# Kernel optimization log

Measured on AMD Instinct MI355X. Metric: run time of the kernel, lower is better.

The kernel has to match this reference:

```python
import jax, jax.numpy as jnp
import numpy as np

N, E = 100000, 3200000
F_NODE, F_EDGE = 2, 7
H, C = 4, 8
HC = H * C
REG, TGT = 500, 1
NUM_LAYERS = 3
ATT_SLOPE = 0.2   # LeakyReLU inside GATv2 attention
ACT_SLOPE = 0.01  # model-level LeakyReLU default
BN_EPS = 1e-5


def gatv2(x, src, dst, e_attr, Wl, bl, Wr, br, We, att, bias):
    n = x.shape[0]
    xl = (x @ Wl + bl).reshape(n, H, C)          # source transform (messages)
    xr = (x @ Wr + br).reshape(n, H, C)          # destination transform
    ee = (e_attr @ We).reshape(-1, H, C)         # edge transform (no bias in PyG)
    m = jax.nn.leaky_relu(xl[src] + xr[dst] + ee, ATT_SLOPE)  # [Ef,H,C]
    logits = jnp.einsum('ehc,hc->eh', m, att)    # [Ef,H]
    mx = jax.ops.segment_max(logits, dst, num_segments=n)
    ex = jnp.exp(logits - mx[dst])
    den = jax.ops.segment_sum(ex, dst, num_segments=n)
    alpha = ex / (den[dst] + 1e-16)              # edge-softmax grouped by dst
    out = jax.ops.segment_sum(xl[src] * alpha[:, :, None], dst, num_segments=n)
    return out.reshape(n, HC) + bias             # concat heads + bias


def setup_inputs() -> dict:
    key = jax.random.key(0)
    ks = jax.random.split(key, 30)
    # edges with no self loops (module calls add_self_loops on top)
    s = jax.random.randint(ks[0], (E,), 0, N, dtype=jnp.int32)
    off = jax.random.randint(ks[1], (E,), 1, N, dtype=jnp.int32)
    d = (s + off) % N
    edge_index = jnp.stack([s, d])
    x = jax.random.normal(ks[2], (N, F_NODE), dtype=jnp.float32)
    edge_attr = jax.random.normal(ks[3], (E, F_EDGE), dtype=jnp.float32)

    def glorot(k, shape):
        fan = shape[0] + shape[-1]
        return jax.random.normal(k, shape, dtype=jnp.float32) * jnp.sqrt(2.0 / fan)

    inp = dict(x=x, edge_index=edge_index, edge_attr=edge_attr)
    i = 4
    for tag, fin in (("1", F_NODE), ("2", HC)):
        inp["Wl" + tag] = glorot(ks[i], (fin, HC)); i += 1
        inp["bl" + tag] = jnp.zeros((HC,), jnp.float32)
        inp["Wr" + tag] = glorot(ks[i], (fin, HC)); i += 1
        inp["br" + tag] = jnp.zeros((HC,), jnp.float32)
        inp["We" + tag] = glorot(ks[i], (F_EDGE, HC)); i += 1
        inp["att" + tag] = glorot(ks[i], (H, C)); i += 1
        inp["b" + tag] = jnp.zeros((HC,), jnp.float32)
    inp["gamma"] = jnp.ones((HC,), jnp.float32)
    inp["beta"] = jnp.zeros((HC,), jnp.float32)
    inp["Wreg"] = glorot(ks[i], (HC, REG)); i += 1
    inp["breg"] = jnp.zeros((REG,), jnp.float32)
    inp["Wend"] = glorot(ks[i], (REG, TGT)); i += 1
    inp["bend"] = jnp.zeros((TGT,), jnp.float32)
    return inp


def reference(x, edge_index, edge_attr,
              Wl1, bl1, Wr1, br1, We1, att1, b1,
              Wl2, bl2, Wr2, br2, We2, att2, b2,
              gamma, beta, Wreg, breg, Wend, bend):
    n = x.shape[0]
    loop = jnp.arange(n, dtype=edge_index.dtype)
    srcf = jnp.concatenate([edge_index[0], loop])
    dstf = jnp.concatenate([edge_index[1], loop])
    # self-loop edge attrs filled with mean (PyG fill_value='mean')
    ea_mean = jnp.mean(edge_attr, axis=0, keepdims=True)
    eaf = jnp.concatenate([edge_attr, jnp.broadcast_to(ea_mean, (n, edge_attr.shape[1]))])

    h = gatv2(x, srcf, dstf, eaf, Wl1, bl1, Wr1, br1, We1, att1, b1)
    for _ in range(NUM_LAYERS - 1):
        mu = jnp.mean(h, axis=0)
        var = jnp.var(h, axis=0)
        h = (h - mu) * jax.lax.rsqrt(var + BN_EPS) * gamma + beta
        h = jax.nn.leaky_relu(h, ACT_SLOPE)
        h = gatv2(h, srcf, dstf, eaf, Wl2, bl2, Wr2, br2, We2, att2, b2)
    h = jax.nn.leaky_relu(h, ACT_SLOPE)
    h = h @ Wreg + breg
    return h @ Wend + bend
```

## Files before the change

kernel.cpp:

```cpp
#include <hip/hip_runtime.h>
#include <hip/hip_fp16.h>
#include <math.h>

#define NN 100000
#define EE 3200000
#define FE 7
#define GNB 32
#define CRR 1280
#define NBK 391
#define BKCAP 8688
#define T1 8192
#define FB1 ((EE + T1 - 1) / T1)

typedef unsigned int uivec4 __attribute__((ext_vector_type(4)));
static __device__ __forceinline__ uint4 ntload4(const uint4* p) {
    uivec4 v = __builtin_nontemporal_load((const uivec4*)p);
    uint4 r; r.x = v.x; r.y = v.y; r.z = v.z; r.w = v.w; return r;
}

static __device__ __forceinline__ __half2 hmax2(__half2 a, __half2 b) {
    unsigned int ua = *(unsigned int*)&a, ub = *(unsigned int*)&b, ur;
    asm("v_pk_max_f16 %0, %1, %2" : "=v"(ur) : "v"(ua), "v"(ub));
    return *(__half2*)&ur;
}


__global__ void k_prep(const float* __restrict__ Wreg, const float* __restrict__ breg,
                       const float* __restrict__ Wend, const float* __restrict__ bend,
                       float* __restrict__ wend, float* __restrict__ c0v,
                       int* __restrict__ gbucket) {
    if (blockIdx.x == 0) {
        int t = threadIdx.x;
        if (t < 32) {
            float s = 0.f;
            for (int k = 0; k < 500; ++k) s = fmaf(Wreg[t * 500 + k], Wend[k], s);
            wend[t] = s;
        } else if (t == 32) {
            float s = 0.f;
            for (int k = 0; k < 500; ++k) s = fmaf(breg[k], Wend[k], s);
            *c0v = s + bend[0];
        }
    } else {
        for (int i = threadIdx.x; i < NBK; i += 256) gbucket[i] = i * BKCAP;
    }
}

__global__ __launch_bounds__(512) void k_fill1(const int* __restrict__ ei,
                                               const float* __restrict__ ea,
                                               int* __restrict__ gbucket,
                                               uint4* __restrict__ srt,
                                               double* __restrict__ ea_sum) {
    __shared__ int hbin[NBK];
    __shared__ float part[8][FE];
    for (int i = threadIdx.x; i < NBK; i += 512) hbin[i] = 0;
    __syncthreads();
    int e0 = blockIdx.x * T1;
    int ecnt = EE - e0; if (ecnt > T1) ecnt = T1;
    for (int i = threadIdx.x; i < ecnt; i += 512) {
        int d = ei[EE + e0 + i];
        atomicAdd(&hbin[d >> 8], 1);
    }
    __syncthreads();
    for (int i = threadIdx.x; i < NBK; i += 512) {
        int c = hbin[i];
        hbin[i] = (c > 0) ? atomicAdd(&gbucket[i], c) : 0;
    }
    __syncthreads();
    float acc[FE];
#pragma unroll
    for (int f = 0; f < FE; ++f) acc[f] = 0.f;
    for (int i = threadIdx.x; i < ecnt; i += 512) {
        int e = e0 + i;
        int d = ei[EE + e];
        int b = d >> 8;
        unsigned dl = (unsigned)(d & 255);
        int pos = atomicAdd(&hbin[b], 1);
        int s = ei[e];
        const float* rr = ea + (size_t)e * FE;
        unsigned h[FE];
#pragma unroll
        for (int f = 0; f < FE; ++f) {
            float af = __builtin_nontemporal_load(rr + f);
            acc[f] += af;
            h[f] = (unsigned)__half_as_ushort(__float2half_rn(af));
        }
#pragma unroll
        for (int f = 0; f < 6; ++f) { h[f] = (h[f] + 1) >> 1; if (h[f] > 0x7FFFu) h[f] = 0x7FFFu; }
        unsigned h6 = (h[6] + 4) >> 3; if (h6 > 0x1FFFu) h6 = 0x1FFFu;
        uint4 u;
        u.x = h[0] | (h[1] << 15) | ((dl & 3u) << 30);
        u.y = h[2] | (h[3] << 15) | (((dl >> 2) & 3u) << 30);
        u.z = h[4] | (h[5] << 15) | (((dl >> 4) & 3u) << 30);
        u.w = (unsigned)s | (h6 << 17) | ((dl >> 6) << 30);
        srt[(size_t)pos] = u;
    }
    int wave = threadIdx.x >> 6;
#pragma unroll
    for (int f = 0; f < FE; ++f) {
        float v = acc[f];
        for (int o = 32; o > 0; o >>= 1) v += __shfl_down(v, o, 64);
        if ((threadIdx.x & 63) == 0) part[wave][f] = v;
    }
    __syncthreads();
    if (threadIdx.x < FE) {
        float s = 0.f;
#pragma unroll
        for (int i = 0; i < 8; ++i) s += part[i][threadIdx.x];
        atomicAdd(&ea_sum[threadIdx.x], (double)s);
    }
}

__global__ __launch_bounds__(512) void k_bscan(const int* __restrict__ gbucket,
                                               int* __restrict__ bbase,
                                               const double* __restrict__ ea_sum,
                                               float* __restrict__ ea_mean) {
    __shared__ int ts[512];
    int t = threadIdx.x;
    if (t < 8) ea_mean[t] = (t < FE) ? (float)(ea_sum[t] / (double)EE) : 0.f;
    int c = (t < NBK) ? (gbucket[t] - t * BKCAP) : 0;
    ts[t] = c;
    __syncthreads();
    for (int o = 1; o < 512; o <<= 1) {
        int u = (t >= o) ? ts[t - o] : 0;
        __syncthreads();
        ts[t] += u;
        __syncthreads();
    }
    if (t < NBK) bbase[t] = ts[t] - c;
}

__global__ __launch_bounds__(512) void k_fill2(const uint4* __restrict__ srt,
                                               const int* __restrict__ gbucket,
                                               const int* __restrict__ bbase,
                                               int* __restrict__ offs,
                                               uint4* __restrict__ rec) {
    __shared__ int hist[256], hcopy[256], strt[256];
    int t = threadIdx.x;
    int b = blockIdx.x;
    int nbase = b << 8;
    int nb = NN - nbase; if (nb > 256) nb = 256;
    int sbase = b * BKCAP;
    int cnt = gbucket[b] - sbase;
    int bb = bbase[b];
    if (t < 256) hist[t] = 0;
    __syncthreads();
    for (int p = t; p < cnt; p += 512) {
        uint4 s = srt[(size_t)(sbase + p)];
        int dl = (int)((s.x >> 30) | ((s.y >> 30) << 2) | ((s.z >> 30) << 4) | ((s.w >> 30) << 6));
        atomicAdd(&hist[dl], 1);
    }
    __syncthreads();
    if (t < 256) hcopy[t] = hist[t];
    __syncthreads();
    for (int o = 1; o < 256; o <<= 1) {
        int u = 0;
        if (t < 256 && t >= o) u = hist[t - o];
        __syncthreads();
        if (t < 256) hist[t] += u;
        __syncthreads();
    }
    if (t < 256) {
        int c = hcopy[t];
        int start = bb + hist[t] - c;
        strt[t] = start;
        if (t < nb) offs[nbase + t] = start + c;
    }
    __syncthreads();
    for (int p = t; p < cnt; p += 512) {
        uint4 s = srt[(size_t)(sbase + p)];
        int dl = (int)((s.x >> 30) | ((s.y >> 30) << 2) | ((s.z >> 30) << 4) | ((s.w >> 30) << 6));
        int pos = atomicAdd(&strt[dl], 1);
        uint4 u;
        u.x = ((s.x & 0x7FFFu) << 1) | (((s.x >> 15) & 0x7FFFu) << 17);
        u.y = ((s.y & 0x7FFFu) << 1) | (((s.y >> 15) & 0x7FFFu) << 17);
        u.z = ((s.z & 0x7FFFu) << 1) | (((s.z >> 15) & 0x7FFFu) << 17);
        u.w = (s.w & 0x1FFFFu) | (((s.w >> 17) & 0x1FFFu) << 19);
        rec[(size_t)pos] = u;
    }
}

template <int FIN, bool BN>
__global__ void k_xform(const float* __restrict__ h,
                        const float* __restrict__ Wl, const float* __restrict__ bl,
                        const float* __restrict__ Wr, const float* __restrict__ br,
                        const double* __restrict__ bn_part, const double* __restrict__ bn_sqpart,
                        const float* __restrict__ gamma, const float* __restrict__ beta,
                        __half* __restrict__ xl, __half* __restrict__ xr) {
    __shared__ float sWl[FIN * 32], sWr[FIN * 32], sb[64];
    __shared__ float smu[FIN], ssc[FIN], sbe[FIN];
    for (int i = threadIdx.x; i < FIN * 32; i += blockDim.x) { sWl[i] = Wl[i]; sWr[i] = Wr[i]; }
    if (threadIdx.x < 32) { sb[threadIdx.x] = bl[threadIdx.x]; sb[32 + threadIdx.x] = br[threadIdx.x]; }
    if (BN && threadIdx.x < FIN) {
        int f = threadIdx.x;
        double s = 0.0, q = 0.0;
#pragma unroll
        for (int k = 0; k < 32; ++k) { s += bn_part[k * 32 + f]; q += bn_sqpart[k * 32 + f]; }
        double mu = s * (1.0 / NN);
        double var = q * (1.0 / NN) - mu * mu;
        smu[f] = (float)mu;
        ssc[f] = gamma[f] * (float)(1.0 / sqrt(var + 1e-5));
        sbe[f] = beta[f];
    }
    __syncthreads();
    int idx = blockIdx.x * blockDim.x + threadIdx.x;
    if (idx >= NN * 32) return;
    int n = idx >> 5, c = idx & 31;
    const float* hr = h + (size_t)n * FIN;
    float al = sb[c], ar = sb[32 + c];
#pragma unroll
    for (int f = 0; f < FIN; ++f) {
        float v = hr[f];
        if (BN) {
            v = fmaf(v - smu[f], ssc[f], sbe[f]);
            v = v > 0.f ? v : 0.01f * v;
        }
        al = fmaf(v, sWl[f * 32 + c], al);
        ar = fmaf(v, sWr[f * 32 + c], ar);
    }
    xl[idx] = __float2half(al);
    xr[idx] = __float2half(ar);
}

template <int MODE>
__global__ __launch_bounds__(256) void k_gat_t(
    const int* __restrict__ offs, const uint4* __restrict__ rec,
    const __half* __restrict__ xl, const __half* __restrict__ xr,
    const float* __restrict__ We, const float* __restrict__ att,
    const float* __restrict__ bias, const float* __restrict__ ea_mean,
    float* __restrict__ hout, double* __restrict__ bn_part,
    double* __restrict__ bn_sqpart, const float* __restrict__ wend,
    const float* __restrict__ c0v, float* __restrict__ out) {
    __shared__ uint4 srec[CRR];
    int n0 = blockIdx.x * GNB;
    int g = threadIdx.x >> 3, j = threadIdx.x & 7, c0 = j * 4;
    int node = n0 + g;

    __half2 weh[FE][2];
#pragma unroll
    for (int f = 0; f < FE; ++f) {
        weh[f][0] = __floats2half2_rn(We[f * 32 + c0], We[f * 32 + c0 + 1]);
        weh[f][1] = __floats2half2_rn(We[f * 32 + c0 + 2], We[f * 32 + c0 + 3]);
    }
    float at0 = att[c0], at1 = att[c0 + 1], at2 = att[c0 + 2], at3 = att[c0 + 3];
    float eam[FE];
#pragma unroll
    for (int f = 0; f < FE; ++f) eam[f] = ea_mean[f];

    float2 rawr = *(const float2*)(xr + (size_t)node * 32 + c0);
    __half2 qh01 = *(const __half2*)&rawr.x;
    __half2 qh23 = *(const __half2*)&rawr.y;
    float2 q01 = __half22float2(qh01);
    float2 q23 = __half22float2(qh23);

    int s_g = (node == 0) ? 0 : offs[node - 1];
    int e_g = offs[node];
    int range0 = (n0 == 0) ? 0 : offs[n0 - 1];
    int range1 = offs[n0 + GNB - 1];

    float sm = 0.f, acc0 = 0.f, acc1 = 0.f, acc2 = 0.f, acc3 = 0.f;
    const __half2 c02 = __float2half2_rn(0.2f);

    auto edge_op = [&](uint4 u, float2 rawl) {
        __half2 lh01 = *(const __half2*)&rawl.x;
        __half2 lh23 = *(const __half2*)&rawl.y;
        __half2 ah01 = *(const __half2*)&u.x;
        __half2 ah23 = *(const __half2*)&u.y;
        __half2 ah45 = *(const __half2*)&u.z;
        __half a6h = __ushort_as_half((unsigned short)((u.w >> 16) & 0xFFFEu));
        __half2 e01 = qh01, e23 = qh23;
        __half2 bc;
        bc = __low2half2(ah01);  e01 = __hfma2(bc, weh[0][0], e01); e23 = __hfma2(bc, weh[0][1], e23);
        bc = __high2half2(ah01); e01 = __hfma2(bc, weh[1][0], e01); e23 = __hfma2(bc, weh[1][1], e23);
        bc = __low2half2(ah23);  e01 = __hfma2(bc, weh[2][0], e01); e23 = __hfma2(bc, weh[2][1], e23);
        bc = __high2half2(ah23); e01 = __hfma2(bc, weh[3][0], e01); e23 = __hfma2(bc, weh[3][1], e23);
        bc = __low2half2(ah45);  e01 = __hfma2(bc, weh[4][0], e01); e23 = __hfma2(bc, weh[4][1], e23);
        bc = __high2half2(ah45); e01 = __hfma2(bc, weh[5][0], e01); e23 = __hfma2(bc, weh[5][1], e23);
        bc = __half2half2(a6h);  e01 = __hfma2(bc, weh[6][0], e01); e23 = __hfma2(bc, weh[6][1], e23);
        __half2 v01 = __hadd2(e01, lh01);
        __half2 v23 = __hadd2(e23, lh23);
        v01 = hmax2(v01, __hmul2(v01, c02));
        v23 = hmax2(v23, __hmul2(v23, c02));
        float2 f01 = __half22float2(v01), f23 = __half22float2(v23);
        float pl = fmaf(f01.x, at0, fmaf(f01.y, at1, fmaf(f23.x, at2, f23.y * at3)));
        float L = pl + __shfl_xor(pl, 1, 64);
        float ex = __expf(L);
        sm += ex;
        float2 l01 = __half22float2(lh01), l23 = __half22float2(lh23);
        acc0 = fmaf(ex, l01.x, acc0);
        acc1 = fmaf(ex, l01.y, acc1);
        acc2 = fmaf(ex, l23.x, acc2);
        acc3 = fmaf(ex, l23.y, acc3);
    };

    for (int base = range0; base < range1; base += CRR) {
        int cnt = range1 - base; if (cnt > CRR) cnt = CRR;
        __syncthreads();
        for (int i = threadIdx.x; i < cnt; i += 256)
            srec[i] = ntload4(&rec[(size_t)base + i]);
        __syncthreads();
        int lo = s_g > base ? s_g : base;
        int hi = e_g < base + cnt ? e_g : base + cnt;
        if (lo >= hi) continue;
        int i1 = lo + 1 < hi ? lo + 1 : hi - 1;
        int i2 = lo + 2 < hi ? lo + 2 : hi - 1;
        uint4 ua = srec[lo - base];
        float2 ra = *(const float2*)(xl + (size_t)(ua.w & 0x1FFFFu) * 32 + c0);
        uint4 ub = srec[i1 - base];
        float2 rb = *(const float2*)(xl + (size_t)(ub.w & 0x1FFFFu) * 32 + c0);
        uint4 uc = srec[i2 - base];
        float2 rc = *(const float2*)(xl + (size_t)(uc.w & 0x1FFFFu) * 32 + c0);
#pragma unroll 3
        for (int p = lo; p < hi; ++p) {
            uint4 cu = ua; float2 cr = ra;
            ua = ub; ra = rb;
            ub = uc; rb = rc;
            int pn = p + 3 < hi ? p + 3 : hi - 1;
            uc = srec[pn - base];
            rc = *(const float2*)(xl + (size_t)(uc.w & 0x1FFFFu) * 32 + c0);
            edge_op(cu, cr);
        }
    }

    {
        float2 rawl = *(const float2*)(xl + (size_t)node * 32 + c0);
        float2 l01 = __half22float2(*(const __half2*)&rawl.x);
        float2 l23 = __half22float2(*(const __half2*)&rawl.y);
        float ee0 = q01.x, ee1 = q01.y, ee2 = q23.x, ee3 = q23.y;
        float wef[FE][4];
#pragma unroll
        for (int f = 0; f < FE; ++f) {
            float2 w0 = __half22float2(weh[f][0]);
            float2 w1 = __half22float2(weh[f][1]);
            wef[f][0] = w0.x; wef[f][1] = w0.y; wef[f][2] = w1.x; wef[f][3] = w1.y;
        }
#pragma unroll
        for (int f = 0; f < FE; ++f) {
            ee0 = fmaf(eam[f], wef[f][0], ee0);
            ee1 = fmaf(eam[f], wef[f][1], ee1);
            ee2 = fmaf(eam[f], wef[f][2], ee2);
            ee3 = fmaf(eam[f], wef[f][3], ee3);
        }
        float v0 = ee0 + l01.x;
        float v1 = ee1 + l01.y;
        float v2 = ee2 + l23.x;
        float v3 = ee3 + l23.y;
        v0 = fmaxf(v0, 0.2f * v0);
        v1 = fmaxf(v1, 0.2f * v1);
        v2 = fmaxf(v2, 0.2f * v2);
        v3 = fmaxf(v3, 0.2f * v3);
        float pl = fmaf(v0, at0, fmaf(v1, at1, fmaf(v2, at2, v3 * at3)));
        float L = pl + __shfl_xor(pl, 1, 64);
        float ex = __expf(L);
        sm += ex;
        acc0 = fmaf(ex, l01.x, acc0);
        acc1 = fmaf(ex, l01.y, acc1);
        acc2 = fmaf(ex, l23.x, acc2);
        acc3 = fmaf(ex, l23.y, acc3);
    }

    float inv = 1.f / (sm + 1e-16f);
    float o0 = fmaf(acc0, inv, bias[c0 + 0]);
    float o1 = fmaf(acc1, inv, bias[c0 + 1]);
    float o2 = fmaf(acc2, inv, bias[c0 + 2]);
    float o3 = fmaf(acc3, inv, bias[c0 + 3]);
    if constexpr (MODE != 2) {
        float4 o; o.x = o0; o.y = o1; o.z = o2; o.w = o3;
        *(float4*)(hout + (size_t)node * 32 + c0) = o;
    }
    if constexpr (MODE == 1) {
        float s0 = o0, s1 = o1, s2 = o2, s3 = o3;
        float z0 = o0 * o0, z1 = o1 * o1, z2 = o2 * o2, z3 = o3 * o3;
#pragma unroll
        for (int off = 8; off < 64; off <<= 1) {
            s0 += __shfl_xor(s0, off, 64); z0 += __shfl_xor(z0, off, 64);
            s1 += __shfl_xor(s1, off, 64); z1 += __shfl_xor(z1, off, 64);
            s2 += __shfl_xor(s2, off, 64); z2 += __shfl_xor(z2, off, 64);
            s3 += __shfl_xor(s3, off, 64); z3 += __shfl_xor(z3, off, 64);
        }
        __syncthreads();
        float* red = (float*)srec;
        int wv = threadIdx.x >> 6, lane = threadIdx.x & 63;
        if (lane < 8) {
            float* r = red + (wv * 8 + lane) * 8;
            r[0] = s0; r[1] = s1; r[2] = s2; r[3] = s3;
            r[4] = z0; r[5] = z1; r[6] = z2; r[7] = z3;
        }
        __syncthreads();
        if (threadIdx.x < 32) {
            int jj = threadIdx.x >> 2, kk = threadIdx.x & 3;
            float ts = 0.f, tq = 0.f;
#pragma unroll
            for (int w2 = 0; w2 < 4; ++w2) {
                ts += red[(w2 * 8 + jj) * 8 + kk];
                tq += red[(w2 * 8 + jj) * 8 + 4 + kk];
            }
            int slot = (blockIdx.x & 31) * 32 + threadIdx.x;
            atomicAdd(&bn_part[slot], (double)ts);
            atomicAdd(&bn_sqpart[slot], (double)tq);
        }
    }
    if constexpr (MODE == 2) {
        float w0 = wend[c0], w1 = wend[c0 + 1], w2 = wend[c0 + 2], w3 = wend[c0 + 3];
        float p0 = o0 > 0.f ? o0 : 0.01f * o0;
        float p1 = o1 > 0.f ? o1 : 0.01f * o1;
        float p2 = o2 > 0.f ? o2 : 0.01f * o2;
        float p3 = o3 > 0.f ? o3 : 0.01f * o3;
        float p = fmaf(p0, w0, fmaf(p1, w1, fmaf(p2, w2, p3 * w3)));
        p += __shfl_xor(p, 1, 64);
        p += __shfl_xor(p, 2, 64);
        p += __shfl_xor(p, 4, 64);
        if (j == 0) out[node] = p + *c0v;
    }
}

extern "C" void kernel_launch(void* const* d_in, const int* in_sizes, int n_in,
                              void* d_out, int out_size, void* d_ws, size_t ws_size,
                              hipStream_t stream) {
    (void)in_sizes; (void)n_in; (void)out_size; (void)ws_size;
    const float* x    = (const float*)d_in[0];
    const int*   ei   = (const int*)d_in[1];
    const float* ea   = (const float*)d_in[2];
    const float* Wl1  = (const float*)d_in[3];
    const float* bl1  = (const float*)d_in[4];
    const float* Wr1  = (const float*)d_in[5];
    const float* br1  = (const float*)d_in[6];
    const float* We1  = (const float*)d_in[7];
    const float* att1 = (const float*)d_in[8];
    const float* b1   = (const float*)d_in[9];
    const float* Wl2  = (const float*)d_in[10];
    const float* bl2  = (const float*)d_in[11];
    const float* Wr2  = (const float*)d_in[12];
    const float* br2  = (const float*)d_in[13];
    const float* We2  = (const float*)d_in[14];
    const float* att2 = (const float*)d_in[15];
    const float* b2   = (const float*)d_in[16];
    const float* gamma= (const float*)d_in[17];
    const float* beta = (const float*)d_in[18];
    const float* Wreg = (const float*)d_in[19];
    const float* breg = (const float*)d_in[20];
    const float* Wend = (const float*)d_in[21];
    const float* bend = (const float*)d_in[22];
    float* out = (float*)d_out;

    char* w = (char*)d_ws;
    double* ea_sum   = (double*)(w + 0);
    float*  ea_mean  = (float*)(w + 576);
    float*  wend     = (float*)(w + 608);
    float*  c0v      = (float*)(w + 736);
    int*    gbucket  = (int*)(w + 2048);
    int*    bbase    = (int*)(w + 4096);
    double* bn_part  = (double*)(w + 8192);
    double* bn_sqp   = (double*)(w + 16384);
    size_t o = 24576;
    int* offs = (int*)(w + o); o += ((size_t)NN * 4 + 255) & ~(size_t)255;
    __half* xl = (__half*)(w + o); o += ((size_t)NN * 32 * 2 + 255) & ~(size_t)255;
    __half* xr = (__half*)(w + o); o += ((size_t)NN * 32 * 2 + 255) & ~(size_t)255;
    float* hb = (float*)(w + o); o += (size_t)NN * 32 * 4;
    uint4* rec = (uint4*)(w + o); o += (size_t)EE * 16;
    uint4* srt = (uint4*)(w + o); o += (size_t)NBK * BKCAP * 16;

    hipMemsetAsync(w, 0, 1024, stream);
    hipMemsetAsync(w + 8192, 0, 16384, stream);

    k_prep<<<2, 256, 0, stream>>>(Wreg, breg, Wend, bend, wend, c0v, gbucket);
    k_fill1<<<FB1, 512, 0, stream>>>(ei, ea, gbucket, srt, ea_sum);
    k_bscan<<<1, 512, 0, stream>>>(gbucket, bbase, ea_sum, ea_mean);
    k_fill2<<<NBK, 512, 0, stream>>>(srt, gbucket, bbase, offs, rec);

    const int xbl = (NN * 32 + 255) / 256;
    const int gbl = NN / GNB;

    k_xform<2, false><<<xbl, 256, 0, stream>>>(x, Wl1, bl1, Wr1, br1,
                                               bn_part, bn_sqp, gamma, beta, xl, xr);
    k_gat_t<1><<<gbl, 256, 0, stream>>>(offs, rec, xl, xr, We1, att1, b1, ea_mean,
                                        hb, bn_part, bn_sqp, wend, c0v, out);

    k_xform<32, true><<<xbl, 256, 0, stream>>>(hb, Wl2, bl2, Wr2, br2,
                                               bn_part, bn_sqp, gamma, beta, xl, xr);
    hipMemsetAsync(w + 8192, 0, 16384, stream);
    k_gat_t<1><<<gbl, 256, 0, stream>>>(offs, rec, xl, xr, We2, att2, b2, ea_mean,
                                        hb, bn_part, bn_sqp, wend, c0v, out);

    k_xform<32, true><<<xbl, 256, 0, stream>>>(hb, Wl2, bl2, Wr2, br2,
                                               bn_part, bn_sqp, gamma, beta, xl, xr);
    k_gat_t<2><<<gbl, 256, 0, stream>>>(offs, rec, xl, xr, We2, att2, b2, ea_mean,
                                        hb, bn_part, bn_sqp, wend, c0v, out);
}
```

Measured before the change: 671.7 us.

## Drop prep kernel and memsets, stage edge attributes through LDS, halve fill tile

Removes k_prep by starting bucket counters at zero, so the bucket base is added inside k_fill1, and by moving the Wreg·Wend reduction into k_bscan. A single memset now zeroes the workspace, and two BN-stat buffers are used so the mid-pipeline memset can go. In k_fill1, edge attributes are loaded into shared memory one coalesced tile of 512 edges at a time with 16-byte nontemporal loads, replacing strided per-thread 4-byte loads. The per-block edge count is halved to T1=4096, which doubles the block count and the global bucket atomics and adds a barrier per tile.

```diff
diff --git a/kernel.cpp b/kernel.cpp
--- a/kernel.cpp
+++ b/kernel.cpp
@@ -9,7 +9,7 @@
 #define CRR 1280
 #define NBK 391
 #define BKCAP 8688
-#define T1 8192
+#define T1 4096
 #define FB1 ((EE + T1 - 1) / T1)
 
 typedef unsigned int uivec4 __attribute__((ext_vector_type(4)));
@@ -24,26 +24,6 @@
     return *(__half2*)&ur;
 }
 
-
-__global__ void k_prep(const float* __restrict__ Wreg, const float* __restrict__ breg,
-                       const float* __restrict__ Wend, const float* __restrict__ bend,
-                       float* __restrict__ wend, float* __restrict__ c0v,
-                       int* __restrict__ gbucket) {
-    if (blockIdx.x == 0) {
-        int t = threadIdx.x;
-        if (t < 32) {
-            float s = 0.f;
-            for (int k = 0; k < 500; ++k) s = fmaf(Wreg[t * 500 + k], Wend[k], s);
-            wend[t] = s;
-        } else if (t == 32) {
-            float s = 0.f;
-            for (int k = 0; k < 500; ++k) s = fmaf(breg[k], Wend[k], s);
-            *c0v = s + bend[0];
-        }
-    } else {
-        for (int i = threadIdx.x; i < NBK; i += 256) gbucket[i] = i * BKCAP;
-    }
-}
 
 __global__ __launch_bounds__(512) void k_fill1(const int* __restrict__ ei,
                                                const float* __restrict__ ea,
@@ -51,36 +31,40 @@
                                                uint4* __restrict__ srt,
                                                double* __restrict__ ea_sum) {
     __shared__ int hbin[NBK];
+    __shared__ uint4 sea[896];
     __shared__ float part[8][FE];
-    for (int i = threadIdx.x; i < NBK; i += 512) hbin[i] = 0;
+    int t = threadIdx.x;
+    for (int i = t; i < NBK; i += 512) hbin[i] = 0;
     __syncthreads();
     int e0 = blockIdx.x * T1;
     int ecnt = EE - e0; if (ecnt > T1) ecnt = T1;
-    for (int i = threadIdx.x; i < ecnt; i += 512) {
-        int d = ei[EE + e0 + i];
-        atomicAdd(&hbin[d >> 8], 1);
-    }
-    __syncthreads();
-    for (int i = threadIdx.x; i < NBK; i += 512) {
+    for (int i = t; i < ecnt; i += 512)
+        atomicAdd(&hbin[ei[EE + e0 + i] >> 8], 1);
+    __syncthreads();
+    for (int i = t; i < NBK; i += 512) {
         int c = hbin[i];
-        hbin[i] = (c > 0) ? atomicAdd(&gbucket[i], c) : 0;
+        hbin[i] = (c > 0) ? (i * BKCAP + atomicAdd(&gbucket[i], c)) : 0;
     }
     __syncthreads();
     float acc[FE];
 #pragma unroll
     for (int f = 0; f < FE; ++f) acc[f] = 0.f;
-    for (int i = threadIdx.x; i < ecnt; i += 512) {
-        int e = e0 + i;
+    for (int tile = 0; tile * 512 < ecnt; ++tile) {
+        int be = e0 + tile * 512;
+        const uint4* gsrc = (const uint4*)(ea + (size_t)be * FE);
+        for (int i = t; i < 896; i += 512) sea[i] = ntload4(&gsrc[i]);
+        __syncthreads();
+        const float* sf = (const float*)sea;
+        int e = be + t;
         int d = ei[EE + e];
         int b = d >> 8;
         unsigned dl = (unsigned)(d & 255);
         int pos = atomicAdd(&hbin[b], 1);
         int s = ei[e];
-        const float* rr = ea + (size_t)e * FE;
         unsigned h[FE];
 #pragma unroll
         for (int f = 0; f < FE; ++f) {
-            float af = __builtin_nontemporal_load(rr + f);
+            float af = sf[t * FE + f];
             acc[f] += af;
             h[f] = (unsigned)__half_as_ushort(__float2half_rn(af));
         }
@@ -93,31 +77,38 @@
         u.z = h[4] | (h[5] << 15) | (((dl >> 4) & 3u) << 30);
         u.w = (unsigned)s | (h6 << 17) | ((dl >> 6) << 30);
         srt[(size_t)pos] = u;
-    }
-    int wave = threadIdx.x >> 6;
+        __syncthreads();
+    }
+    int wave = t >> 6;
 #pragma unroll
     for (int f = 0; f < FE; ++f) {
         float v = acc[f];
         for (int o = 32; o > 0; o >>= 1) v += __shfl_down(v, o, 64);
-        if ((threadIdx.x & 63) == 0) part[wave][f] = v;
-    }
-    __syncthreads();
-    if (threadIdx.x < FE) {
+        if ((t & 63) == 0) part[wave][f] = v;
+    }
+    __syncthreads();
+    if (t < FE) {
         float s = 0.f;
 #pragma unroll
-        for (int i = 0; i < 8; ++i) s += part[i][threadIdx.x];
-        atomicAdd(&ea_sum[threadIdx.x], (double)s);
+        for (int i = 0; i < 8; ++i) s += part[i][t];
+        atomicAdd(&ea_sum[t], (double)s);
     }
 }
 
 __global__ __launch_bounds__(512) void k_bscan(const int* __restrict__ gbucket,
                                                int* __restrict__ bbase,
                                                const double* __restrict__ ea_sum,
-                                               float* __restrict__ ea_mean) {
+                                               float* __restrict__ ea_mean,
+                                               const float* __restrict__ Wreg,
+                                               const float* __restrict__ breg,
+                                               const float* __restrict__ Wend,
+                                               const float* __restrict__ bend,
+                                               float* __restrict__ wend,
+                                               float* __restrict__ c0v) {
     __shared__ int ts[512];
     int t = threadIdx.x;
     if (t < 8) ea_mean[t] = (t < FE) ? (float)(ea_sum[t] / (double)EE) : 0.f;
-    int c = (t < NBK) ? (gbucket[t] - t * BKCAP) : 0;
+    int c = (t < NBK) ? gbucket[t] : 0;
     ts[t] = c;
     __syncthreads();
     for (int o = 1; o < 512; o <<= 1) {
@@ -127,6 +118,16 @@
         __syncthreads();
     }
     if (t < NBK) bbase[t] = ts[t] - c;
+    if (t >= 416 && t < 448) {
+        int r = t - 416;
+        float s = 0.f;
+        for (int k = 0; k < 500; ++k) s = fmaf(Wreg[r * 500 + k], Wend[k], s);
+        wend[r] = s;
+    } else if (t == 448) {
+        float s = 0.f;
+        for (int k = 0; k < 500; ++k) s = fmaf(breg[k], Wend[k], s);
+        *c0v = s + bend[0];
+    }
 }
 
 __global__ __launch_bounds__(512) void k_fill2(const uint4* __restrict__ srt,
@@ -140,7 +141,7 @@
     int nbase = b << 8;
     int nb = NN - nbase; if (nb > 256) nb = 256;
     int sbase = b * BKCAP;
-    int cnt = gbucket[b] - sbase;
+    int cnt = gbucket[b];
     int bb = bbase[b];
     if (t < 256) hist[t] = 0;
     __syncthreads();
@@ -449,9 +450,11 @@
     float*  c0v      = (float*)(w + 736);
     int*    gbucket  = (int*)(w + 2048);
     int*    bbase    = (int*)(w + 4096);
-    double* bn_part  = (double*)(w + 8192);
-    double* bn_sqp   = (double*)(w + 16384);
-    size_t o = 24576;
+    double* bnA_part = (double*)(w + 8192);
+    double* bnA_sqp  = (double*)(w + 16384);
+    double* bnB_part = (double*)(w + 24576);
+    double* bnB_sqp  = (double*)(w + 32768);
+    size_t o = 40960;
     int* offs = (int*)(w + o); o += ((size_t)NN * 4 + 255) & ~(size_t)255;
     __half* xl = (__half*)(w + o); o += ((size_t)NN * 32 * 2 + 255) & ~(size_t)255;
     __half* xr = (__half*)(w + o); o += ((size_t)NN * 32 * 2 + 255) & ~(size_t)255;
@@ -459,30 +462,28 @@
     uint4* rec = (uint4*)(w + o); o += (size_t)EE * 16;
     uint4* srt = (uint4*)(w + o); o += (size_t)NBK * BKCAP * 16;
 
-    hipMemsetAsync(w, 0, 1024, stream);
-    hipMemsetAsync(w + 8192, 0, 16384, stream);
-
-    k_prep<<<2, 256, 0, stream>>>(Wreg, breg, Wend, bend, wend, c0v, gbucket);
+    hipMemsetAsync(w, 0, 40960, stream);
+
     k_fill1<<<FB1, 512, 0, stream>>>(ei, ea, gbucket, srt, ea_sum);
-    k_bscan<<<1, 512, 0, stream>>>(gbucket, bbase, ea_sum, ea_mean);
+    k_bscan<<<1, 512, 0, stream>>>(gbucket, bbase, ea_sum, ea_mean,
+                                   Wreg, breg, Wend, bend, wend, c0v);
     k_fill2<<<NBK, 512, 0, stream>>>(srt, gbucket, bbase, offs, rec);
 
     const int xbl = (NN * 32 + 255) / 256;
     const int gbl = NN / GNB;
 
     k_xform<2, false><<<xbl, 256, 0, stream>>>(x, Wl1, bl1, Wr1, br1,
-                                               bn_part, bn_sqp, gamma, beta, xl, xr);
+                                               bnA_part, bnA_sqp, gamma, beta, xl, xr);
     k_gat_t<1><<<gbl, 256, 0, stream>>>(offs, rec, xl, xr, We1, att1, b1, ea_mean,
-                                        hb, bn_part, bn_sqp, wend, c0v, out);
+                                        hb, bnA_part, bnA_sqp, wend, c0v, out);
 
     k_xform<32, true><<<xbl, 256, 0, stream>>>(hb, Wl2, bl2, Wr2, br2,
-                                               bn_part, bn_sqp, gamma, beta, xl, xr);
-    hipMemsetAsync(w + 8192, 0, 16384, stream);
+                                               bnA_part, bnA_sqp, gamma, beta, xl, xr);
     k_gat_t<1><<<gbl, 256, 0, stream>>>(offs, rec, xl, xr, We2, att2, b2, ea_mean,
-                                        hb, bn_part, bn_sqp, wend, c0v, out);
+                                        hb, bnB_part, bnB_sqp, wend, c0v, out);
 
     k_xform<32, true><<<xbl, 256, 0, stream>>>(hb, Wl2, bl2, Wr2, br2,
-                                               bn_part, bn_sqp, gamma, beta, xl, xr);
+                                               bnB_part, bnB_sqp, gamma, beta, xl, xr);
     k_gat_t<2><<<gbl, 256, 0, stream>>>(offs, rec, xl, xr, We2, att2, b2, ea_mean,
-                                        hb, bn_part, bn_sqp, wend, c0v, out);
-}
+                                        hb, bnA_part, bnA_sqp, wend, c0v, out);
+}
```

Measured after the change: 648.9 us. -3.4%, faster.
